# Kernel optimization log

Hardware: AMD Instinct MI355X
Metric: run time of the kernel (lower is better)

The kernel has to match this reference:

```python
import math
import jax, jax.numpy as jnp
import numpy as np

N_HEADS = 16

def setup_inputs() -> dict:
    key = jax.random.key(0)
    qkv = jax.random.normal(key, (4, 3072, 2048), dtype=jnp.float32)
    return {"qkv": qkv}

def reference(qkv):
    bs, width, length = qkv.shape
    ch = width // (3 * N_HEADS)
    # [bs*H, 3*ch, L] -> split into q, k, v of [bs*H, ch, L]
    qkv_r = qkv.reshape(bs * N_HEADS, 3 * ch, length)
    q, k, v = qkv_r[:, :ch], qkv_r[:, ch:2 * ch], qkv_r[:, 2 * ch:]
    scale = 1.0 / math.sqrt(math.sqrt(ch))
    # scores: [bs*H, T, S]
    weight = jnp.einsum('bct,bcs->bts', q * scale, k * scale)
    weight = jax.nn.softmax(weight, axis=-1)
    a = jnp.einsum('bts,bcs->bct', weight, v)
    return a.reshape(bs, -1, length)
```

## Files before the change

### kernel.cpp

```cpp
#include <hip/hip_runtime.h>
#include <cstdint>

typedef _Float16 half8 __attribute__((ext_vector_type(8)));
typedef __fp16 fp16x2 __attribute__((ext_vector_type(2)));
typedef float f32x4 __attribute__((ext_vector_type(4)));

#define HSTRIDE 131072
#define KOFF    ((size_t)64 * HSTRIDE)
#define VOFF    ((size_t)128 * HSTRIDE)

__device__ __forceinline__ float fast_exp2(float x) {
    return __builtin_amdgcn_exp2f(x);
}

__device__ __forceinline__ uint32_t pkrtz(float a, float b) {
    fp16x2 h = __builtin_amdgcn_cvt_pkrtz(a, b);
    return __builtin_bit_cast(uint32_t, h);
}

__device__ __forceinline__ void load_lds16(const _Float16* g, _Float16* l) {
    auto* g1 = reinterpret_cast<const __attribute__((address_space(1))) uint32_t*>(
        reinterpret_cast<uintptr_t>(g));
    auto* l3 = reinterpret_cast<__attribute__((address_space(3))) uint32_t*>(
        reinterpret_cast<uintptr_t>(l));
    __builtin_amdgcn_global_load_lds(g1, l3, 16, 0, 0);
}

__global__ __launch_bounds__(256) void prep_kernel(const float* __restrict__ qkv,
                                                   _Float16* __restrict__ ws)
{
    __shared__ float Lf[64 * 67];

    const int tid  = threadIdx.x;
    const int lane = tid & 63;
    const int wave = tid >> 6;
    const int bid  = blockIdx.x;

    if (bid < 2048) {
        const int head  = (bid >> 5) & 63;
        const int chunk = bid & 31;
        const int b4 = head >> 4, h = head & 15;
        const float* src = qkv + (((size_t)(b4 * 3072 + h * 192 + 64)) << 11)
                         + chunk * 64;

#pragma unroll
        for (int k = 0; k < 4; ++k) {
            int idx = k * 256 + tid;
            int c = idx >> 4;
            int t4 = (idx & 15) << 2;
            float4 f = *(const float4*)&src[(((size_t)c) << 11) + t4];
            float* d = &Lf[c * 67 + t4];
            d[0] = f.x; d[1] = f.y; d[2] = f.z; d[3] = f.w;
        }
        __syncthreads();

        const int q = lane >> 4, l15 = lane & 15;
        const int scol = wave * 16 + l15;
#pragma unroll
        for (int k = 0; k < 2; ++k) {
            uint32_t d[4];
#pragma unroll
            for (int j = 0; j < 4; ++j) {
                float a = Lf[(32 * k + 8 * q + 2 * j) * 67 + scol];
                float b = Lf[(32 * k + 8 * q + 2 * j + 1) * 67 + scol];
                d[j] = pkrtz(a, b);
            }
            size_t off = KOFF + (size_t)head * HSTRIDE
                       + (size_t)((((chunk * 4 + wave) * 2 + k) * 512) + lane * 8);
            *(uint4*)&ws[off] = make_uint4(d[0], d[1], d[2], d[3]);
        }
    } else {
        const int vb = bid - 2048;
        const int head = vb >> 5, chunk = vb & 31;
        const int b4 = head >> 4, h = head & 15;
        const float* src = qkv + (((size_t)(b4 * 3072 + h * 192 + 128)) << 11) + chunk * 64;
        const int q = lane >> 4, cl = lane & 15;
        const int c = wave * 16 + cl;
#pragma unroll
        for (int k = 0; k < 2; ++k) {
            const float* p = &src[((size_t)c << 11) + k * 32 + q * 4];
            float4 f0 = *(const float4*)&p[0];
            float4 f1 = *(const float4*)&p[16];
            size_t off = VOFF + (size_t)head * HSTRIDE
                       + (size_t)(((chunk * 2 + k) * 4 + wave) * 512 + lane * 8);
            *(uint4*)&ws[off] = make_uint4(pkrtz(f0.x, f0.y), pkrtz(f0.z, f0.w),
                                           pkrtz(f1.x, f1.y), pkrtz(f1.z, f1.w));
        }
    }
}

__launch_bounds__(256, 2)
__global__ void attn_kernel(const float* __restrict__ qkv,
                            const _Float16* __restrict__ ws, float* __restrict__ out)
{
    __shared__ __align__(16) _Float16 sK[3][4096];
    __shared__ __align__(16) _Float16 sV[3][4096];

    const int tid  = threadIdx.x;
    const int lane = tid & 63;
    const int wave = tid >> 6;
    const int l15  = lane & 15;
    const int quad = lane >> 4;

    const int bid  = blockIdx.x;
    const int head = bid & 63;
    const int tblk = bid >> 6;
    const int T0   = tblk * 256;
    const int b4   = head >> 4;
    const int h    = head & 15;

    const _Float16* Kt = ws + KOFF + (size_t)head * HSTRIDE;
    const _Float16* Vt = ws + VOFF + (size_t)head * HSTRIDE;
    const float*    Qg = qkv + ((size_t)(b4 * 3072 + h * 192) << 11);
    const float kQ = 0.125f * 1.44269504088896340736f;

    f32x4 Oacc[4][4];
#pragma unroll
    for (int ct = 0; ct < 4; ++ct)
#pragma unroll
        for (int nt = 0; nt < 4; ++nt) Oacc[ct][nt] = (f32x4)0.f;
    float lacc[4] = {0.f, 0.f, 0.f, 0.f};
    const f32x4 fz = (f32x4)0.f;

    auto stage = [&](int buf, int tile) {
        const _Float16* kg = Kt + (size_t)tile * 4096 + wave * 1024 + lane * 8;
        const _Float16* vg = Vt + (size_t)tile * 4096 + wave * 1024 + lane * 8;
        load_lds16(kg,       &sK[buf][wave * 1024]);
        load_lds16(kg + 512, &sK[buf][wave * 1024 + 512]);
        load_lds16(vg,       &sV[buf][wave * 1024]);
        load_lds16(vg + 512, &sV[buf][wave * 1024 + 512]);
    };

    stage(0, 0);

    half8 qb[4][2];
#pragma unroll
    for (int nt = 0; nt < 4; ++nt) {
        const int t = T0 + wave * 64 + nt * 16 + l15;
#pragma unroll
        for (int ks = 0; ks < 2; ++ks) {
            float f[8];
#pragma unroll
            for (int j = 0; j < 8; ++j)
                f[j] = Qg[((size_t)(ks * 32 + quad * 8 + j) << 11) + t];
            uint4 u = make_uint4(pkrtz(f[0] * kQ, f[1] * kQ), pkrtz(f[2] * kQ, f[3] * kQ),
                                 pkrtz(f[4] * kQ, f[5] * kQ), pkrtz(f[6] * kQ, f[7] * kQ));
            qb[nt][ks] = __builtin_bit_cast(half8, u);
        }
    }

    int cur = 0, nxt = 1;
    for (int it = 0; it < 32; ++it) {
        __builtin_amdgcn_s_waitcnt(0);
        __syncthreads();
        if (it < 31) stage(nxt, it + 1);
        const _Float16* sKb = sK[cur];
        const _Float16* sVb = sV[cur];
        cur = nxt; nxt = (nxt == 2) ? 0 : nxt + 1;
        const int lb = lane * 8;

        half8 kf[4][2];
#pragma unroll
        for (int mt = 0; mt < 4; ++mt)
#pragma unroll
            for (int ks = 0; ks < 2; ++ks)
                kf[mt][ks] = *(const half8*)&sKb[(mt * 2 + ks) * 512 + lb];

        half8 pf[2][4];
#pragma unroll
        for (int sc2 = 0; sc2 < 2; ++sc2) {
            f32x4 Sa[4], Sb[4];
#pragma unroll
            for (int nt = 0; nt < 4; ++nt) {
                f32x4 t0 = __builtin_amdgcn_mfma_f32_16x16x32_f16(kf[2 * sc2][0], qb[nt][0], fz, 0, 0, 0);
                Sa[nt]   = __builtin_amdgcn_mfma_f32_16x16x32_f16(kf[2 * sc2][1], qb[nt][1], t0, 0, 0, 0);
                f32x4 t1 = __builtin_amdgcn_mfma_f32_16x16x32_f16(kf[2 * sc2 + 1][0], qb[nt][0], fz, 0, 0, 0);
                Sb[nt]   = __builtin_amdgcn_mfma_f32_16x16x32_f16(kf[2 * sc2 + 1][1], qb[nt][1], t1, 0, 0, 0);
            }
#pragma unroll
            for (int nt = 0; nt < 4; ++nt) {
                float e0 = fast_exp2(Sa[nt][0]);
                float e1 = fast_exp2(Sa[nt][1]);
                float e2 = fast_exp2(Sa[nt][2]);
                float e3 = fast_exp2(Sa[nt][3]);
                float e4 = fast_exp2(Sb[nt][0]);
                float e5 = fast_exp2(Sb[nt][1]);
                float e6 = fast_exp2(Sb[nt][2]);
                float e7 = fast_exp2(Sb[nt][3]);
                lacc[nt] += ((e0 + e1) + (e2 + e3)) + ((e4 + e5) + (e6 + e7));
                uint4 u = make_uint4(pkrtz(e0, e1), pkrtz(e2, e3),
                                     pkrtz(e4, e5), pkrtz(e6, e7));
                pf[sc2][nt] = __builtin_bit_cast(half8, u);
            }
        }

        half8 vf[2][4];
#pragma unroll
        for (int sc2 = 0; sc2 < 2; ++sc2)
#pragma unroll
            for (int ct = 0; ct < 4; ++ct)
                vf[sc2][ct] = *(const half8*)&sVb[(sc2 * 4 + ct) * 512 + lb];
#pragma unroll
        for (int ct = 0; ct < 4; ++ct)
#pragma unroll
            for (int sc2 = 0; sc2 < 2; ++sc2)
#pragma unroll
                for (int nt = 0; nt < 4; ++nt)
                    Oacc[ct][nt] = __builtin_amdgcn_mfma_f32_16x16x32_f16(
                        vf[sc2][ct], pf[sc2][nt], Oacc[ct][nt], 0, 0, 0);
    }

    float inv[4];
#pragma unroll
    for (int nt = 0; nt < 4; ++nt) {
        float v = lacc[nt];
        v += __shfl_xor(v, 16, 64);
        v += __shfl_xor(v, 32, 64);
        inv[nt] = 1.f / v;
    }

    float* ob = out + (((size_t)(b4 * 1024 + h * 64)) << 11) + T0 + wave * 64;
#pragma unroll
    for (int ct = 0; ct < 4; ++ct)
#pragma unroll
        for (int nt = 0; nt < 4; ++nt) {
            f32x4 o = Oacc[ct][nt];
#pragma unroll
            for (int r = 0; r < 4; ++r)
                ob[((size_t)(ct * 16 + quad * 4 + r) << 11) + nt * 16 + l15] = o[r] * inv[nt];
        }
}

extern "C" void kernel_launch(void* const* d_in, const int* in_sizes, int n_in,
                              void* d_out, int out_size, void* d_ws, size_t ws_size,
                              hipStream_t stream) {
    const float* qkv = (const float*)d_in[0];
    float* out = (float*)d_out;
    _Float16* ws = (_Float16*)d_ws;
    prep_kernel<<<dim3(4096), dim3(256), 0, stream>>>(qkv, ws);
    attn_kernel<<<dim3(512), dim3(256), 0, stream>>>(qkv, ws, out);
}
```

Baseline: 218.0 us.

## Software-pipeline S and O stages and compute row sums via MFMA with ones

Restructures the main loop so the PV MFMA for tile i runs alongside the QK/exp work for tile i+1, and prefetches two tiles ahead in the triple-buffered LDS. The softmax denominator is now accumulated with an extra MFMA against a ones vector, replacing the scalar adds and the cross-lane shuffles. This moves VALU reduction work onto the matrix units and lets MFMA and exp instructions interleave, at the cost of more MFMA issues and longer live ranges for the P registers. It also adds a no-op multiply-by-zero term in the V conversion, which looks like a compiler-scheduling tweak.

```diff
diff --git a/kernel.cpp b/kernel.cpp
--- a/kernel.cpp
+++ b/kernel.cpp
@@ -84,7 +84,7 @@
             size_t off = VOFF + (size_t)head * HSTRIDE
                        + (size_t)(((chunk * 2 + k) * 4 + wave) * 512 + lane * 8);
             *(uint4*)&ws[off] = make_uint4(pkrtz(f0.x, f0.y), pkrtz(f0.z, f0.w),
-                                           pkrtz(f1.x, f1.y), pkrtz(f1.z, f1.w));
+                                           pkrtz(f1.x, f1.y), pkrtz(f1.x * 0.f + f1.z, f1.w));
         }
     }
 }
@@ -119,8 +119,16 @@
     for (int ct = 0; ct < 4; ++ct)
 #pragma unroll
         for (int nt = 0; nt < 4; ++nt) Oacc[ct][nt] = (f32x4)0.f;
-    float lacc[4] = {0.f, 0.f, 0.f, 0.f};
+    f32x4 Lacc[4];
+#pragma unroll
+    for (int nt = 0; nt < 4; ++nt) Lacc[nt] = (f32x4)0.f;
     const f32x4 fz = (f32x4)0.f;
+
+    half8 ones;
+#pragma unroll
+    for (int j = 0; j < 8; ++j) ones[j] = (_Float16)1.0f;
+
+    const int lb = lane * 8;
 
     auto stage = [&](int buf, int tile) {
         const _Float16* kg = Kt + (size_t)tile * 4096 + wave * 1024 + lane * 8;
@@ -132,6 +140,7 @@
     };
 
     stage(0, 0);
+    stage(1, 1);
 
     half8 qb[4][2];
 #pragma unroll
@@ -149,24 +158,15 @@
         }
     }
 
-    int cur = 0, nxt = 1;
-    for (int it = 0; it < 32; ++it) {
-        __builtin_amdgcn_s_waitcnt(0);
-        __syncthreads();
-        if (it < 31) stage(nxt, it + 1);
-        const _Float16* sKb = sK[cur];
-        const _Float16* sVb = sV[cur];
-        cur = nxt; nxt = (nxt == 2) ? 0 : nxt + 1;
-        const int lb = lane * 8;
-
+    half8 pf[2][4];
+
+    auto computeS = [&](const _Float16* sKb) {
         half8 kf[4][2];
 #pragma unroll
         for (int mt = 0; mt < 4; ++mt)
 #pragma unroll
             for (int ks = 0; ks < 2; ++ks)
                 kf[mt][ks] = *(const half8*)&sKb[(mt * 2 + ks) * 512 + lb];
-
-        half8 pf[2][4];
 #pragma unroll
         for (int sc2 = 0; sc2 < 2; ++sc2) {
             f32x4 Sa[4], Sb[4];
@@ -187,13 +187,14 @@
                 float e5 = fast_exp2(Sb[nt][1]);
                 float e6 = fast_exp2(Sb[nt][2]);
                 float e7 = fast_exp2(Sb[nt][3]);
-                lacc[nt] += ((e0 + e1) + (e2 + e3)) + ((e4 + e5) + (e6 + e7));
                 uint4 u = make_uint4(pkrtz(e0, e1), pkrtz(e2, e3),
                                      pkrtz(e4, e5), pkrtz(e6, e7));
                 pf[sc2][nt] = __builtin_bit_cast(half8, u);
             }
         }
-
+    };
+
+    auto computeO = [&](const _Float16* sVb) {
         half8 vf[2][4];
 #pragma unroll
         for (int sc2 = 0; sc2 < 2; ++sc2)
@@ -208,16 +209,37 @@
                 for (int nt = 0; nt < 4; ++nt)
                     Oacc[ct][nt] = __builtin_amdgcn_mfma_f32_16x16x32_f16(
                         vf[sc2][ct], pf[sc2][nt], Oacc[ct][nt], 0, 0, 0);
+#pragma unroll
+        for (int sc2 = 0; sc2 < 2; ++sc2)
+#pragma unroll
+            for (int nt = 0; nt < 4; ++nt)
+                Lacc[nt] = __builtin_amdgcn_mfma_f32_16x16x32_f16(
+                    ones, pf[sc2][nt], Lacc[nt], 0, 0, 0);
+    };
+
+    __builtin_amdgcn_s_waitcnt(0);
+    __syncthreads();
+    computeS(sK[0]);
+
+    int bV = 0;
+    for (int it = 0; it < 31; ++it) {
+        __builtin_amdgcn_s_waitcnt(0);
+        __syncthreads();
+        if (it < 30) {
+            int bs_ = bV + 2; if (bs_ >= 3) bs_ -= 3;
+            stage(bs_, it + 2);
+        }
+        int bK = bV + 1; if (bK >= 3) bK -= 3;
+        computeO(sV[bV]);
+        computeS(sK[bK]);
+        bV = bK;
     }
 
+    computeO(sV[bV]);
+
     float inv[4];
 #pragma unroll
-    for (int nt = 0; nt < 4; ++nt) {
-        float v = lacc[nt];
-        v += __shfl_xor(v, 16, 64);
-        v += __shfl_xor(v, 32, 64);
-        inv[nt] = 1.f / v;
-    }
+    for (int nt = 0; nt < 4; ++nt) inv[nt] = 1.f / Lacc[nt][0];
 
     float* ob = out + (((size_t)(b4 * 1024 + h * 64)) << 11) + T0 + wave * 64;
 #pragma unroll
```

After: 213.5 us. 1.02x faster.

## Load K/V fragments directly to registers with software-pipelined skewed loop

Applied to the files above, without the earlier changes.

Drops the LDS triple-buffer staging and block-wide barriers, so each wave loads its K and V fragments straight from global memory into registers, double-buffered one 32-key step ahead. The loop is skewed so the PV MFMAs of the previous step overlap the QK MFMAs and exp of the current step. The row-sum is now computed with an MFMA against a ones vector instead of VALU adds and cross-lane shuffles. In exchange, every wave fetches the K/V tiles from global/L2 separately instead of sharing them through LDS, and register pressure rises.

```diff
diff --git a/kernel.cpp b/kernel.cpp
--- a/kernel.cpp
+++ b/kernel.cpp
@@ -16,14 +16,6 @@
 __device__ __forceinline__ uint32_t pkrtz(float a, float b) {
     fp16x2 h = __builtin_amdgcn_cvt_pkrtz(a, b);
     return __builtin_bit_cast(uint32_t, h);
-}
-
-__device__ __forceinline__ void load_lds16(const _Float16* g, _Float16* l) {
-    auto* g1 = reinterpret_cast<const __attribute__((address_space(1))) uint32_t*>(
-        reinterpret_cast<uintptr_t>(g));
-    auto* l3 = reinterpret_cast<__attribute__((address_space(3))) uint32_t*>(
-        reinterpret_cast<uintptr_t>(l));
-    __builtin_amdgcn_global_load_lds(g1, l3, 16, 0, 0);
 }
 
 __global__ __launch_bounds__(256) void prep_kernel(const float* __restrict__ qkv,
@@ -93,9 +85,6 @@
 __global__ void attn_kernel(const float* __restrict__ qkv,
                             const _Float16* __restrict__ ws, float* __restrict__ out)
 {
-    __shared__ __align__(16) _Float16 sK[3][4096];
-    __shared__ __align__(16) _Float16 sV[3][4096];
-
     const int tid  = threadIdx.x;
     const int lane = tid & 63;
     const int wave = tid >> 6;
@@ -109,8 +98,8 @@
     const int b4   = head >> 4;
     const int h    = head & 15;
 
-    const _Float16* Kt = ws + KOFF + (size_t)head * HSTRIDE;
-    const _Float16* Vt = ws + VOFF + (size_t)head * HSTRIDE;
+    const _Float16* Kt = ws + KOFF + (size_t)head * HSTRIDE + lane * 8;
+    const _Float16* Vt = ws + VOFF + (size_t)head * HSTRIDE + lane * 8;
     const float*    Qg = qkv + ((size_t)(b4 * 3072 + h * 192) << 11);
     const float kQ = 0.125f * 1.44269504088896340736f;
 
@@ -119,19 +108,29 @@
     for (int ct = 0; ct < 4; ++ct)
 #pragma unroll
         for (int nt = 0; nt < 4; ++nt) Oacc[ct][nt] = (f32x4)0.f;
-    float lacc[4] = {0.f, 0.f, 0.f, 0.f};
+    f32x4 Lacc[4];
+#pragma unroll
+    for (int nt = 0; nt < 4; ++nt) Lacc[nt] = (f32x4)0.f;
     const f32x4 fz = (f32x4)0.f;
 
-    auto stage = [&](int buf, int tile) {
-        const _Float16* kg = Kt + (size_t)tile * 4096 + wave * 1024 + lane * 8;
-        const _Float16* vg = Vt + (size_t)tile * 4096 + wave * 1024 + lane * 8;
-        load_lds16(kg,       &sK[buf][wave * 1024]);
-        load_lds16(kg + 512, &sK[buf][wave * 1024 + 512]);
-        load_lds16(vg,       &sV[buf][wave * 1024]);
-        load_lds16(vg + 512, &sV[buf][wave * 1024 + 512]);
-    };
-
-    stage(0, 0);
+    half8 ones;
+#pragma unroll
+    for (int j = 0; j < 8; ++j) ones[j] = (_Float16)1.0f;
+
+    half8 kfA[2][2], kfB[2][2], vfA[4], vfB[4];
+
+#pragma unroll
+    for (int st = 0; st < 2; ++st)
+#pragma unroll
+        for (int ks = 0; ks < 2; ++ks) {
+            kfA[st][ks] = *(const half8*)(Kt + (size_t)(0 * 4 + st * 2 + ks) * 512);
+            kfB[st][ks] = *(const half8*)(Kt + (size_t)(1 * 4 + st * 2 + ks) * 512);
+        }
+#pragma unroll
+    for (int ct = 0; ct < 4; ++ct) {
+        vfA[ct] = *(const half8*)(Vt + (size_t)(0 * 4 + ct) * 512);
+        vfB[ct] = *(const half8*)(Vt + (size_t)(1 * 4 + ct) * 512);
+    }
 
     half8 qb[4][2];
 #pragma unroll
@@ -149,75 +148,87 @@
         }
     }
 
-    int cur = 0, nxt = 1;
-    for (int it = 0; it < 32; ++it) {
-        __builtin_amdgcn_s_waitcnt(0);
-        __syncthreads();
-        if (it < 31) stage(nxt, it + 1);
-        const _Float16* sKb = sK[cur];
-        const _Float16* sVb = sV[cur];
-        cur = nxt; nxt = (nxt == 2) ? 0 : nxt + 1;
-        const int lb = lane * 8;
-
-        half8 kf[4][2];
-#pragma unroll
-        for (int mt = 0; mt < 4; ++mt)
-#pragma unroll
-            for (int ks = 0; ks < 2; ++ks)
-                kf[mt][ks] = *(const half8*)&sKb[(mt * 2 + ks) * 512 + lb];
-
-        half8 pf[2][4];
-#pragma unroll
-        for (int sc2 = 0; sc2 < 2; ++sc2) {
-            f32x4 Sa[4], Sb[4];
-#pragma unroll
-            for (int nt = 0; nt < 4; ++nt) {
-                f32x4 t0 = __builtin_amdgcn_mfma_f32_16x16x32_f16(kf[2 * sc2][0], qb[nt][0], fz, 0, 0, 0);
-                Sa[nt]   = __builtin_amdgcn_mfma_f32_16x16x32_f16(kf[2 * sc2][1], qb[nt][1], t0, 0, 0, 0);
-                f32x4 t1 = __builtin_amdgcn_mfma_f32_16x16x32_f16(kf[2 * sc2 + 1][0], qb[nt][0], fz, 0, 0, 0);
-                Sb[nt]   = __builtin_amdgcn_mfma_f32_16x16x32_f16(kf[2 * sc2 + 1][1], qb[nt][1], t1, 0, 0, 0);
-            }
-#pragma unroll
-            for (int nt = 0; nt < 4; ++nt) {
-                float e0 = fast_exp2(Sa[nt][0]);
-                float e1 = fast_exp2(Sa[nt][1]);
-                float e2 = fast_exp2(Sa[nt][2]);
-                float e3 = fast_exp2(Sa[nt][3]);
-                float e4 = fast_exp2(Sb[nt][0]);
-                float e5 = fast_exp2(Sb[nt][1]);
-                float e6 = fast_exp2(Sb[nt][2]);
-                float e7 = fast_exp2(Sb[nt][3]);
-                lacc[nt] += ((e0 + e1) + (e2 + e3)) + ((e4 + e5) + (e6 + e7));
-                uint4 u = make_uint4(pkrtz(e0, e1), pkrtz(e2, e3),
-                                     pkrtz(e4, e5), pkrtz(e6, e7));
-                pf[sc2][nt] = __builtin_bit_cast(half8, u);
-            }
-        }
-
-        half8 vf[2][4];
-#pragma unroll
-        for (int sc2 = 0; sc2 < 2; ++sc2)
+    half8 pf[4];
+
+    {
+        f32x4 Sa[4], Sb[4];
+#pragma unroll
+        for (int nt = 0; nt < 4; ++nt) {
+            f32x4 t0 = __builtin_amdgcn_mfma_f32_16x16x32_f16(kfA[0][0], qb[nt][0], fz, 0, 0, 0);
+            Sa[nt]   = __builtin_amdgcn_mfma_f32_16x16x32_f16(kfA[0][1], qb[nt][1], t0, 0, 0, 0);
+            f32x4 t1 = __builtin_amdgcn_mfma_f32_16x16x32_f16(kfA[1][0], qb[nt][0], fz, 0, 0, 0);
+            Sb[nt]   = __builtin_amdgcn_mfma_f32_16x16x32_f16(kfA[1][1], qb[nt][1], t1, 0, 0, 0);
+        }
+#pragma unroll
+        for (int nt = 0; nt < 4; ++nt) {
+            uint4 u = make_uint4(pkrtz(fast_exp2(Sa[nt][0]), fast_exp2(Sa[nt][1])),
+                                 pkrtz(fast_exp2(Sa[nt][2]), fast_exp2(Sa[nt][3])),
+                                 pkrtz(fast_exp2(Sb[nt][0]), fast_exp2(Sb[nt][1])),
+                                 pkrtz(fast_exp2(Sb[nt][2]), fast_exp2(Sb[nt][3])));
+            pf[nt] = __builtin_bit_cast(half8, u);
+        }
+    }
+
+    auto body = [&](int i, half8 (&kfC)[2][2], half8 (&kfN)[2][2],
+                    half8 (&vfN)[4], bool pre) {
+        if (pre) {
+#pragma unroll
+            for (int st = 0; st < 2; ++st)
+#pragma unroll
+                for (int ks = 0; ks < 2; ++ks)
+                    kfN[st][ks] = *(const half8*)(Kt + (size_t)((i + 1) * 4 + st * 2 + ks) * 512);
+        }
+#pragma unroll
+        for (int ct = 0; ct < 4; ++ct)
+#pragma unroll
+            for (int nt = 0; nt < 4; ++nt)
+                Oacc[ct][nt] = __builtin_amdgcn_mfma_f32_16x16x32_f16(
+                    vfN[ct], pf[nt], Oacc[ct][nt], 0, 0, 0);
+#pragma unroll
+        for (int nt = 0; nt < 4; ++nt)
+            Lacc[nt] = __builtin_amdgcn_mfma_f32_16x16x32_f16(ones, pf[nt], Lacc[nt], 0, 0, 0);
+        if (pre) {
 #pragma unroll
             for (int ct = 0; ct < 4; ++ct)
-                vf[sc2][ct] = *(const half8*)&sVb[(sc2 * 4 + ct) * 512 + lb];
-#pragma unroll
-        for (int ct = 0; ct < 4; ++ct)
-#pragma unroll
-            for (int sc2 = 0; sc2 < 2; ++sc2)
-#pragma unroll
-                for (int nt = 0; nt < 4; ++nt)
-                    Oacc[ct][nt] = __builtin_amdgcn_mfma_f32_16x16x32_f16(
-                        vf[sc2][ct], pf[sc2][nt], Oacc[ct][nt], 0, 0, 0);
-    }
+                vfN[ct] = *(const half8*)(Vt + (size_t)((i + 1) * 4 + ct) * 512);
+        }
+        f32x4 Sa[4], Sb[4];
+#pragma unroll
+        for (int nt = 0; nt < 4; ++nt) {
+            f32x4 t0 = __builtin_amdgcn_mfma_f32_16x16x32_f16(kfC[0][0], qb[nt][0], fz, 0, 0, 0);
+            Sa[nt]   = __builtin_amdgcn_mfma_f32_16x16x32_f16(kfC[0][1], qb[nt][1], t0, 0, 0, 0);
+            f32x4 t1 = __builtin_amdgcn_mfma_f32_16x16x32_f16(kfC[1][0], qb[nt][0], fz, 0, 0, 0);
+            Sb[nt]   = __builtin_amdgcn_mfma_f32_16x16x32_f16(kfC[1][1], qb[nt][1], t1, 0, 0, 0);
+        }
+#pragma unroll
+        for (int nt = 0; nt < 4; ++nt) {
+            uint4 u = make_uint4(pkrtz(fast_exp2(Sa[nt][0]), fast_exp2(Sa[nt][1])),
+                                 pkrtz(fast_exp2(Sa[nt][2]), fast_exp2(Sa[nt][3])),
+                                 pkrtz(fast_exp2(Sb[nt][0]), fast_exp2(Sb[nt][1])),
+                                 pkrtz(fast_exp2(Sb[nt][2]), fast_exp2(Sb[nt][3])));
+            pf[nt] = __builtin_bit_cast(half8, u);
+        }
+    };
+
+    for (int m = 0; m < 31; ++m) {
+        body(2 * m + 1, kfB, kfA, vfA, true);
+        body(2 * m + 2, kfA, kfB, vfB, true);
+    }
+    body(63, kfB, kfA, vfA, false);
+
+#pragma unroll
+    for (int ct = 0; ct < 4; ++ct)
+#pragma unroll
+        for (int nt = 0; nt < 4; ++nt)
+            Oacc[ct][nt] = __builtin_amdgcn_mfma_f32_16x16x32_f16(
+                vfB[ct], pf[nt], Oacc[ct][nt], 0, 0, 0);
+#pragma unroll
+    for (int nt = 0; nt < 4; ++nt)
+        Lacc[nt] = __builtin_amdgcn_mfma_f32_16x16x32_f16(ones, pf[nt], Lacc[nt], 0, 0, 0);
 
     float inv[4];
 #pragma unroll
-    for (int nt = 0; nt < 4; ++nt) {
-        float v = lacc[nt];
-        v += __shfl_xor(v, 16, 64);
-        v += __shfl_xor(v, 32, 64);
-        inv[nt] = 1.f / v;
-    }
+    for (int nt = 0; nt < 4; ++nt) inv[nt] = 1.f / Lacc[nt][0];
 
     float* ob = out + (((size_t)(b4 * 1024 + h * 64)) << 11) + T0 + wave * 64;
 #pragma unroll
```

After: 215.9 us. Within noise of the previous version (-1.0%).
